# Optimization experiments

Hardware: AMD Instinct MI355X
Metric: run time of the kernel (lower is better)

Reference implementation:

```python
import jax, jax.numpy as jnp
import numpy as np

S, B, D, H, HD = 2048, 4, 1280, 16, 80  # seq, batch, d_model, heads, head_dim
NSEG = 8


def setup_inputs() -> dict:
    key = jax.random.key(0)
    k0, k1, k2 = jax.random.split(key, 3)
    x = jax.random.normal(k0, (S, B, D), dtype=jnp.float32)
    Wqkv = jax.random.normal(k1, (D, 3 * D), dtype=jnp.float32) * 0.02
    bqkv = jnp.zeros((3 * D,), dtype=jnp.float32)
    Wproj = jax.random.normal(k2, (D, 4 * D), dtype=jnp.float32) * 0.02
    bproj = jnp.zeros((4 * D,), dtype=jnp.float32)
    # 8 equal windows of 256 tokens: [0, 256, 512, ..., 2048]
    cu_seqlens = (jnp.arange(NSEG + 1, dtype=jnp.int32) * (S // NSEG))
    return {"x": x, "Wqkv": Wqkv, "bqkv": bqkv, "Wproj": Wproj,
            "bproj": bproj, "cu_seqlens": cu_seqlens}


def reference(x, Wqkv, bqkv, Wproj, bproj, cu_seqlens):
    s, b, d = x.shape
    qkv = x @ Wqkv + bqkv                     # [s, b, 3d]
    q, k, v = jnp.split(qkv, 3, axis=2)       # each [s, b, d]
    def to_bhsd(t):
        return t.reshape(s, b, H, HD).transpose(1, 2, 0, 3)  # [b, h, s, hd]
    q, k, v = to_bhsd(q), to_bhsd(k), to_bhsd(v)
    # Block-diagonal mask: token t belongs to window searchsorted(cu[1:], t, right)
    pos = jnp.arange(s)
    seg = jnp.searchsorted(cu_seqlens[1:], pos, side='right')  # [s]
    bias = jnp.where(seg[:, None] == seg[None, :], 0.0,
                     jnp.finfo(x.dtype).min)                   # [s, s]
    scale = 1.0 / jnp.sqrt(jnp.asarray(HD, dtype=x.dtype))
    scores = jnp.einsum('bhsd,bhtd->bhst', q, k) * scale + bias
    attn = jax.nn.softmax(scores, axis=-1)
    out = jnp.einsum('bhst,bhtd->bhsd', attn, v)               # [b, h, s, hd]
    context = out.transpose(2, 0, 1, 3).reshape(s, b, H * HD)  # [s, b, d]
    return context @ Wproj + bproj                             # [s, b, 4d]
```

## Files before the change

kernel.cpp:

```cpp
#include <hip/hip_runtime.h>

typedef _Float16 f16;
typedef _Float16 f16x8 __attribute__((ext_vector_type(8)));
typedef _Float16 f16x4 __attribute__((ext_vector_type(4)));
typedef float    f32x4 __attribute__((ext_vector_type(4)));
typedef unsigned int u32t;

#define AS1 __attribute__((address_space(1)))
#define AS3 __attribute__((address_space(3)))

static __device__ __forceinline__ void gload_lds16(const void* g, void* l) {
  __builtin_amdgcn_global_load_lds((const AS1 u32t*)g, (AS3 u32t*)l, 16, 0, 0);
}

static __device__ __forceinline__ f16x8 zero8() {
  f16x8 z;
#pragma unroll
  for (int j = 0; j < 8; ++j) z[j] = (f16)0;
  return z;
}

__global__ void k_cvt_x(const float* __restrict__ in, f16* __restrict__ out, int n4) {
  int stride = gridDim.x * blockDim.x;
  for (int i = blockIdx.x * blockDim.x + threadIdx.x; i < n4; i += stride) {
    float4 v = ((const float4*)in)[i];
    f16x4 o;
    o[0] = (f16)v.x; o[1] = (f16)v.y; o[2] = (f16)v.z; o[3] = (f16)v.w;
    ((f16x4*)out)[i] = o;
  }
}

__global__ void k_cvt_w_t(const float* __restrict__ W, f16* __restrict__ Wt, int N) {
  __shared__ float T[32][33];
  int bk = blockIdx.x % 40;
  int bn = blockIdx.x / 40;
  int k0 = bk * 32, n0 = bn * 32;
  int r = threadIdx.x >> 5;
  int c = threadIdx.x & 31;
#pragma unroll
  for (int i = 0; i < 4; ++i)
    T[r + i * 8][c] = W[(size_t)(k0 + r + i * 8) * N + n0 + c];
  __syncthreads();
#pragma unroll
  for (int i = 0; i < 4; ++i)
    Wt[(size_t)(n0 + r + i * 8) * 1280 + k0 + c] = (f16)T[c][r + i * 8];
}

template<int NCOLS, bool F16OUT>
__global__ __launch_bounds__(256, 2)
void gemm_nt(const f16* __restrict__ A, const f16* __restrict__ Bt,
             const float* __restrict__ bias, void* __restrict__ Cout)
{
  __shared__ __align__(16) f16 sA[128 * 64];
  __shared__ __align__(16) f16 sB[128 * 64];
  const int tid = threadIdx.x;
  const int wave = tid >> 6, lane = tid & 63;
  constexpr int NBN = NCOLS / 128;
  const int bm = blockIdx.x / NBN, bn = blockIdx.x % NBN;
  const long row0 = (long)bm * 128, col0 = (long)bn * 128;

  f32x4 acc[4][4];
#pragma unroll
  for (int i = 0; i < 4; ++i)
#pragma unroll
    for (int j = 0; j < 4; ++j) acc[i][j] = (f32x4){0.f, 0.f, 0.f, 0.f};

  const int wr = (wave >> 1) * 64, wc = (wave & 1) * 64;

  int segr[4], segoff[4];
#pragma unroll
  for (int i = 0; i < 4; ++i) {
    int o = (wave * 4 + i) * 1024 + lane * 16;
    int r = o >> 7, cb = o & 127;
    segr[i] = r;
    segoff[i] = cb ^ ((r & 7) << 4);
  }

  const char* Ab = (const char*)A;
  const char* Bb = (const char*)Bt;

  for (int kt = 0; kt < 20; ++kt) {
    __syncthreads();
#pragma unroll
    for (int i = 0; i < 4; ++i) {
      const char* ga = Ab + ((row0 + segr[i]) * 1280 + kt * 64) * 2 + segoff[i];
      gload_lds16(ga, (char*)sA + (wave * 4 + i) * 1024);
      const char* gb = Bb + ((col0 + segr[i]) * 1280 + kt * 64) * 2 + segoff[i];
      gload_lds16(gb, (char*)sB + (wave * 4 + i) * 1024);
    }
    __syncthreads();

#pragma unroll
    for (int kk = 0; kk < 2; ++kk) {
      const int rl = lane & 15, g = lane >> 4, x7 = lane & 7;
      const int ph = (kk * 4 + g) ^ x7;
      f16x8 af[4], bf[4];
#pragma unroll
      for (int mt = 0; mt < 4; ++mt)
        af[mt] = *(const f16x8*)(sA + (wr + mt * 16 + rl) * 64 + ph * 8);
#pragma unroll
      for (int nt = 0; nt < 4; ++nt)
        bf[nt] = *(const f16x8*)(sB + (wc + nt * 16 + rl) * 64 + ph * 8);
#pragma unroll
      for (int mt = 0; mt < 4; ++mt)
#pragma unroll
        for (int nt = 0; nt < 4; ++nt)
          acc[mt][nt] = __builtin_amdgcn_mfma_f32_16x16x32_f16(af[mt], bf[nt], acc[mt][nt], 0, 0, 0);
    }
  }

  const int rl = lane & 15, g = lane >> 4;
#pragma unroll
  for (int mt = 0; mt < 4; ++mt) {
#pragma unroll
    for (int nt = 0; nt < 4; ++nt) {
      long c = col0 + wc + nt * 16 + rl;
      float bv = bias[c];
#pragma unroll
      for (int r = 0; r < 4; ++r) {
        long rr = row0 + wr + mt * 16 + g * 4 + r;
        float v = acc[mt][nt][r] + bv;
        if (F16OUT) ((f16*)Cout)[rr * NCOLS + c] = (f16)v;
        else        ((float*)Cout)[rr * NCOLS + c] = v;
      }
    }
  }
}

__global__ void k_vt(const f16* __restrict__ qkv, f16* __restrict__ vt) {
  __shared__ __align__(16) f16 T[128 * 136];
  int bid = blockIdx.x;
  int sc16 = bid & 15, bh = bid >> 4;
  int b = bh >> 4, h = bh & 15;
  int s0 = sc16 * 128;
  int t = threadIdx.x;
#pragma unroll
  for (int i = 0; i < 5; ++i) {
    int cid = i * 256 + t;
    int s = cid / 10, c = cid % 10;
    const f16* g = qkv + (size_t)((s0 + s) * 4 + b) * 3840 + 2560 + h * 80 + c * 8;
    f16x8 v = *(const f16x8*)g;
    int phys = c ^ ((s >> 3) & 7);
    *(f16x8*)(T + s * 136 + phys * 8) = v;
  }
  __syncthreads();
#pragma unroll
  for (int i = 0; i < 5; ++i) {
    int oid = i * 256 + t;
    int sc8 = oid & 15, hd = oid >> 4;
    f16x8 o;
#pragma unroll
    for (int j = 0; j < 8; ++j) {
      int row = sc8 * 8 + j;
      int phys = (hd >> 3) ^ (sc8 & 7);
      o[j] = T[row * 136 + phys * 8 + (hd & 7)];
    }
    *(f16x8*)(vt + (size_t)(bh * 80 + hd) * 2048 + s0 + sc8 * 8) = o;
  }
}

__global__ __launch_bounds__(512, 2)
void k_attn(const f16* __restrict__ qkv, const f16* __restrict__ vt,
            f16* __restrict__ ctx)
{
  __shared__ __align__(16) f16 sK[256 * 104];
  __shared__ __align__(16) f16 sV[80 * 264];
  __shared__ __align__(16) f16 sP[128 * 72];

  const int bid = blockIdx.x;
  const int qc = bid & 1, seg = (bid >> 1) & 7, h = (bid >> 4) & 15, b = bid >> 8;
  const int t = threadIdx.x;
  const int wave = t >> 6, lane = t & 63;
  const int s_key0 = seg * 256;

#pragma unroll
  for (int i = 0; i < 5; ++i) {
    int cid = i * 512 + t;
    int key = cid / 10, c = cid % 10;
    const f16* g = qkv + (size_t)((s_key0 + key) * 4 + b) * 3840 + 1280 + h * 80 + c * 8;
    *(f16x8*)(sK + key * 104 + c * 8) = *(const f16x8*)g;
  }
  {
    int key = t >> 1, c = t & 1;
    *(f16x8*)(sK + key * 104 + 80 + c * 8) = zero8();
  }
#pragma unroll
  for (int i = 0; i < 5; ++i) {
    int cid = i * 512 + t;
    int hd = cid >> 5, c = cid & 31;
    const f16* g = vt + (size_t)((b * 16 + h) * 80 + hd) * 2048 + s_key0 + c * 8;
    *(f16x8*)(sV + hd * 264 + c * 8) = *(const f16x8*)g;
  }

  const int q0 = s_key0 + qc * 128 + wave * 16;
  const int rl = lane & 15, g = lane >> 4;
  f16x8 qf[3];
  {
    const f16* gq = qkv + (size_t)((q0 + rl) * 4 + b) * 3840 + h * 80;
    qf[0] = *(const f16x8*)(gq + g * 8);
    qf[1] = *(const f16x8*)(gq + 32 + g * 8);
    if (g < 2) qf[2] = *(const f16x8*)(gq + 64 + g * 8);
    else       qf[2] = zero8();
  }
  __syncthreads();

  f32x4 sc[16];
#pragma unroll
  for (int nt = 0; nt < 16; ++nt) sc[nt] = (f32x4){0.f, 0.f, 0.f, 0.f};
#pragma unroll
  for (int nt = 0; nt < 16; ++nt) {
#pragma unroll
    for (int kk = 0; kk < 3; ++kk) {
      f16x8 bf = *(const f16x8*)(sK + (nt * 16 + rl) * 104 + kk * 32 + g * 8);
      sc[nt] = __builtin_amdgcn_mfma_f32_16x16x32_f16(qf[kk], bf, sc[nt], 0, 0, 0);
    }
  }

  const float scale = 0.11180339887498949f;
  float inv[4];
#pragma unroll
  for (int r = 0; r < 4; ++r) {
    float m = -1e30f;
#pragma unroll
    for (int nt = 0; nt < 16; ++nt) m = fmaxf(m, sc[nt][r]);
#pragma unroll
    for (int off = 8; off >= 1; off >>= 1) m = fmaxf(m, __shfl_xor(m, off));
    m *= scale;
    float sum = 0.f;
#pragma unroll
    for (int nt = 0; nt < 16; ++nt) {
      float p = __expf(sc[nt][r] * scale - m);
      sc[nt][r] = p;
      sum += p;
    }
#pragma unroll
    for (int off = 8; off >= 1; off >>= 1) sum += __shfl_xor(sum, off);
    inv[r] = 1.0f / sum;
  }

  f32x4 o[5];
#pragma unroll
  for (int nt = 0; nt < 5; ++nt) o[nt] = (f32x4){0.f, 0.f, 0.f, 0.f};
  const int prow0 = wave * 16;
  for (int ch = 0; ch < 4; ++ch) {
    __syncthreads();
#pragma unroll
    for (int f = 0; f < 4; ++f) {
      int nt = ch * 4 + f;
#pragma unroll
      for (int r = 0; r < 4; ++r)
        sP[(prow0 + g * 4 + r) * 72 + f * 16 + rl] = (f16)sc[nt][r];
    }
    __syncthreads();
#pragma unroll
    for (int kk = 0; kk < 2; ++kk) {
      f16x8 pa = *(const f16x8*)(sP + (prow0 + rl) * 72 + kk * 32 + g * 8);
#pragma unroll
      for (int nt = 0; nt < 5; ++nt) {
        f16x8 vb = *(const f16x8*)(sV + (nt * 16 + rl) * 264 + ch * 64 + kk * 32 + g * 8);
        o[nt] = __builtin_amdgcn_mfma_f32_16x16x32_f16(pa, vb, o[nt], 0, 0, 0);
      }
    }
  }

#pragma unroll
  for (int nt = 0; nt < 5; ++nt) {
    int hd = nt * 16 + rl;
#pragma unroll
    for (int r = 0; r < 4; ++r) {
      long qrow = q0 + g * 4 + r;
      float v = o[nt][r] * inv[r];
      ctx[(qrow * 4 + b) * 1280 + h * 80 + hd] = (f16)v;
    }
  }
}

extern "C" void kernel_launch(void* const* d_in, const int* in_sizes, int n_in,
                              void* d_out, int out_size, void* d_ws, size_t ws_size,
                              hipStream_t stream)
{
  const float* x     = (const float*)d_in[0];
  const float* Wqkv  = (const float*)d_in[1];
  const float* bqkv  = (const float*)d_in[2];
  const float* Wproj = (const float*)d_in[3];
  const float* bproj = (const float*)d_in[4];

  char* ws = (char*)d_ws;
  f16* X16   = (f16*)(ws);
  f16* WQT   = (f16*)(ws + 20971520);
  f16* WPT   = (f16*)(ws + 30801920);
  f16* QKV16 = (f16*)(ws + 43909120);
  f16* VT    = (f16*)(ws + 106823680);
  f16* CTX16 = X16;

  k_cvt_x<<<4096, 256, 0, stream>>>(x, X16, 8192 * 1280 / 4);
  k_cvt_w_t<<<40 * 120, 256, 0, stream>>>(Wqkv, WQT, 3840);
  k_cvt_w_t<<<40 * 160, 256, 0, stream>>>(Wproj, WPT, 5120);
  gemm_nt<3840, true ><<<64 * 30, 256, 0, stream>>>(X16, WQT, bqkv, QKV16);
  k_vt<<<1024, 256, 0, stream>>>(QKV16, VT);
  k_attn<<<1024, 512, 0, stream>>>(QKV16, VT, CTX16);
  gemm_nt<5120, false><<<64 * 40, 256, 0, stream>>>(CTX16, WPT, bproj, d_out);
}
```

Measured before the change: 285.8 us.

## Rework GEMM with 32x32 MFMA, XCD-aware block remap, LDS-staged epilogue; drop attention syncs

The GEMM kernel moves from 16x16x32 MFMA tiles to 32x32x16 tiles with per-wave 2x2 fragments. It also remaps block IDs so neighbouring tiles land on the same XCD, and raises wave priority around the MFMA block. The epilogue now stages results through swizzled LDS so global stores are coalesced vector writes instead of scattered scalars. Separately, the attention kernel drops two __syncthreads around the per-wave P buffer, which is safe because each wave only touches its own rows, though it relies on the compiler keeping the LDS write/read order.

```diff
diff --git a/kernel.cpp b/kernel.cpp
--- a/kernel.cpp
+++ b/kernel.cpp
@@ -4,6 +4,7 @@
 typedef _Float16 f16x8 __attribute__((ext_vector_type(8)));
 typedef _Float16 f16x4 __attribute__((ext_vector_type(4)));
 typedef float    f32x4 __attribute__((ext_vector_type(4)));
+typedef float    f32x16 __attribute__((ext_vector_type(16)));
 typedef unsigned int u32t;
 
 #define AS1 __attribute__((address_space(1)))
@@ -46,26 +47,27 @@
     Wt[(size_t)(n0 + r + i * 8) * 1280 + k0 + c] = (f16)T[c][r + i * 8];
 }
 
+
 template<int NCOLS, bool F16OUT>
 __global__ __launch_bounds__(256, 2)
 void gemm_nt(const f16* __restrict__ A, const f16* __restrict__ Bt,
              const float* __restrict__ bias, void* __restrict__ Cout)
 {
-  __shared__ __align__(16) f16 sA[128 * 64];
-  __shared__ __align__(16) f16 sB[128 * 64];
+  __shared__ __align__(16) char lds[32768];
+  char* const sA = lds;
+  char* const sB = lds + 16384;
+
   const int tid = threadIdx.x;
   const int wave = tid >> 6, lane = tid & 63;
+  const int x7 = lane & 7, l5 = lane >> 5, r31 = lane & 31;
+  const int wm = wave >> 1, wn = wave & 1;
+
   constexpr int NBN = NCOLS / 128;
-  const int bm = blockIdx.x / NBN, bn = blockIdx.x % NBN;
+  constexpr int NWG = 64 * NBN;
+  const int bid = blockIdx.x;
+  const int wgid = (bid & 7) * (NWG / 8) + (bid >> 3);
+  const int bm = wgid / NBN, bn = wgid % NBN;
   const long row0 = (long)bm * 128, col0 = (long)bn * 128;
-
-  f32x4 acc[4][4];
-#pragma unroll
-  for (int i = 0; i < 4; ++i)
-#pragma unroll
-    for (int j = 0; j < 4; ++j) acc[i][j] = (f32x4){0.f, 0.f, 0.f, 0.f};
-
-  const int wr = (wave >> 1) * 64, wc = (wave & 1) * 64;
 
   int segr[4], segoff[4];
 #pragma unroll
@@ -75,53 +77,89 @@
     segr[i] = r;
     segoff[i] = cb ^ ((r & 7) << 4);
   }
-
   const char* Ab = (const char*)A;
   const char* Bb = (const char*)Bt;
 
+  int offA[2], offB[2], kchunk[4];
+#pragma unroll
+  for (int f = 0; f < 2; ++f) {
+    offA[f] = (wm * 64 + f * 32 + r31) << 7;
+    offB[f] = (wn * 64 + f * 32 + r31) << 7;
+  }
+#pragma unroll
+  for (int ks = 0; ks < 4; ++ks) kchunk[ks] = ((ks * 2 + l5) ^ x7) << 4;
+
+  f32x16 acc[2][2];
+#pragma unroll
+  for (int i = 0; i < 2; ++i)
+#pragma unroll
+    for (int j = 0; j < 2; ++j)
+#pragma unroll
+      for (int r = 0; r < 16; ++r) acc[i][j][r] = 0.f;
+
   for (int kt = 0; kt < 20; ++kt) {
     __syncthreads();
 #pragma unroll
     for (int i = 0; i < 4; ++i) {
       const char* ga = Ab + ((row0 + segr[i]) * 1280 + kt * 64) * 2 + segoff[i];
-      gload_lds16(ga, (char*)sA + (wave * 4 + i) * 1024);
+      gload_lds16(ga, sA + (wave * 4 + i) * 1024);
       const char* gb = Bb + ((col0 + segr[i]) * 1280 + kt * 64) * 2 + segoff[i];
-      gload_lds16(gb, (char*)sB + (wave * 4 + i) * 1024);
+      gload_lds16(gb, sB + (wave * 4 + i) * 1024);
     }
     __syncthreads();
 
-#pragma unroll
-    for (int kk = 0; kk < 2; ++kk) {
-      const int rl = lane & 15, g = lane >> 4, x7 = lane & 7;
-      const int ph = (kk * 4 + g) ^ x7;
-      f16x8 af[4], bf[4];
-#pragma unroll
-      for (int mt = 0; mt < 4; ++mt)
-        af[mt] = *(const f16x8*)(sA + (wr + mt * 16 + rl) * 64 + ph * 8);
-#pragma unroll
-      for (int nt = 0; nt < 4; ++nt)
-        bf[nt] = *(const f16x8*)(sB + (wc + nt * 16 + rl) * 64 + ph * 8);
-#pragma unroll
-      for (int mt = 0; mt < 4; ++mt)
-#pragma unroll
-        for (int nt = 0; nt < 4; ++nt)
-          acc[mt][nt] = __builtin_amdgcn_mfma_f32_16x16x32_f16(af[mt], bf[nt], acc[mt][nt], 0, 0, 0);
-    }
-  }
-
-  const int rl = lane & 15, g = lane >> 4;
-#pragma unroll
-  for (int mt = 0; mt < 4; ++mt) {
-#pragma unroll
-    for (int nt = 0; nt < 4; ++nt) {
-      long c = col0 + wc + nt * 16 + rl;
-      float bv = bias[c];
-#pragma unroll
-      for (int r = 0; r < 4; ++r) {
-        long rr = row0 + wr + mt * 16 + g * 4 + r;
-        float v = acc[mt][nt][r] + bv;
-        if (F16OUT) ((f16*)Cout)[rr * NCOLS + c] = (f16)v;
-        else        ((float*)Cout)[rr * NCOLS + c] = v;
+    f16x8 af[2][4], bf[2][4];
+#pragma unroll
+    for (int f = 0; f < 2; ++f)
+#pragma unroll
+      for (int ks = 0; ks < 4; ++ks) {
+        af[f][ks] = *(const f16x8*)(sA + offA[f] + kchunk[ks]);
+        bf[f][ks] = *(const f16x8*)(sB + offB[f] + kchunk[ks]);
+      }
+    __builtin_amdgcn_s_setprio(1);
+#pragma unroll
+    for (int ks = 0; ks < 4; ++ks)
+#pragma unroll
+      for (int mf = 0; mf < 2; ++mf)
+#pragma unroll
+        for (int nf = 0; nf < 2; ++nf)
+          acc[mf][nf] = __builtin_amdgcn_mfma_f32_32x32x16_f16(
+              af[mf][ks], bf[nf][ks], acc[mf][nf], 0, 0, 0);
+    __builtin_amdgcn_s_setprio(0);
+  }
+
+  float* bb = (float*)lds;
+  const int cc0 = wn * 64 + r31;
+  const float bv0 = bias[col0 + cc0];
+  const float bv1 = bias[col0 + cc0 + 32];
+  const int lrow_rd = tid >> 2, qc = tid & 3;
+  const long grow_base = row0 + (lrow_rd >> 5) * 64 + (lrow_rd & 31);
+
+#pragma unroll
+  for (int mf = 0; mf < 2; ++mf) {
+    __syncthreads();
+#pragma unroll
+    for (int nf = 0; nf < 2; ++nf) {
+      const int cc = cc0 + nf * 32;
+      const float bv = nf ? bv1 : bv0;
+#pragma unroll
+      for (int r = 0; r < 16; ++r) {
+        int lrow = wm * 32 + (r & 3) + 8 * (r >> 2) + 4 * l5;
+        bb[lrow * 128 + (((cc >> 2) ^ (lrow & 7)) << 2) + (cc & 3)] = acc[mf][nf][r] + bv;
+      }
+    }
+    __syncthreads();
+    const long grow = grow_base + mf * 32;
+#pragma unroll
+    for (int i = 0; i < 8; ++i) {
+      int ch = qc * 8 + i;
+      f32x4 v = *(const f32x4*)(bb + lrow_rd * 128 + ((ch ^ (lrow_rd & 7)) << 2));
+      long c = col0 + ch * 4;
+      if (F16OUT) {
+        f16x4 h; h[0] = (f16)v[0]; h[1] = (f16)v[1]; h[2] = (f16)v[2]; h[3] = (f16)v[3];
+        *(f16x4*)((f16*)Cout + grow * NCOLS + c) = h;
+      } else {
+        *(f32x4*)((float*)Cout + grow * NCOLS + c) = v;
       }
     }
   }
@@ -243,7 +281,6 @@
   for (int nt = 0; nt < 5; ++nt) o[nt] = (f32x4){0.f, 0.f, 0.f, 0.f};
   const int prow0 = wave * 16;
   for (int ch = 0; ch < 4; ++ch) {
-    __syncthreads();
 #pragma unroll
     for (int f = 0; f < 4; ++f) {
       int nt = ch * 4 + f;
@@ -251,7 +288,6 @@
       for (int r = 0; r < 4; ++r)
         sP[(prow0 + g * 4 + r) * 72 + f * 16 + rl] = (f16)sc[nt][r];
     }
-    __syncthreads();
 #pragma unroll
     for (int kk = 0; kk < 2; ++kk) {
       f16x8 pa = *(const f16x8*)(sP + (prow0 + rl) * 72 + kk * 32 + g * 8);
```

Result: slower. 358.7 us (+25.5%).
